# Kernel optimization log

Hardware: AMD Instinct MI355X
Metric: run time of the kernel (lower is better)

Reference implementation:

```python
import jax, jax.numpy as jnp
import numpy as np

BS, H, W, A, NC, G = 2048, 14, 14, 5, 2, 30
SIZE = 1 + NC + 4  # conf, classes, x, y, w, h
OBJ_SCALE, NOOBJ_SCALE, CLASS_SCALE, COORD_SCALE = 5.0, 0.5, 1.0, 1.0


def setup_inputs() -> dict:
    key = jax.random.key(0)
    pred = jax.random.normal(key, (BS, A * SIZE, H, W), dtype=jnp.float32) * 0.5
    # Structured label: G ground-truth boxes per image at distinct cells.
    rng = np.random.default_rng(0)
    lab = np.zeros((BS, 7, H, W), np.float32)
    perm = np.argsort(rng.random((BS, H * W)), axis=1)[:, :G]  # distinct cells
    r, c = perm // W, perm % W
    b = np.arange(BS)[:, None]
    lab[b, 0, r, c] = 1.0
    cls = rng.integers(0, 2, (BS, G)).astype(np.float32)
    lab[b, 1, r, c] = cls
    lab[b, 2, r, c] = 1.0 - cls
    lab[b, 3, r, c] = rng.uniform(0.1, 0.9, (BS, G))  # tx in-cell offset
    lab[b, 4, r, c] = rng.uniform(0.1, 0.9, (BS, G))  # ty
    lab[b, 5, r, c] = rng.uniform(0.05, 0.4, (BS, G))  # tw (normalized)
    lab[b, 6, r, c] = rng.uniform(0.05, 0.4, (BS, G))  # th
    anchors = np.array([[42.0, 44.0], [91.0, 104.0], [162.0, 220.0],
                        [299.0, 170.0], [396.0, 359.0]], np.float32)
    return {"pred": pred, "label": jnp.asarray(lab),
            "anchors": jnp.asarray(anchors), "seen": 6400}


def _yolo_v2_loss(pred, label, anchors, seen):
    f32 = jnp.float32
    anchor_bias = anchors / (512.0 / 14.0) / jnp.array([W, H], f32)  # [A,2], grid-normalized
    # [BS,H,W,A,SIZE]
    pred_r = pred.transpose(0, 2, 3, 1).reshape(BS, H, W, A, SIZE)
    sxy = jax.nn.sigmoid(pred_r[..., 1 + NC:3 + NC])               # sigmoid(x,y)
    ids = jnp.stack(jnp.meshgrid(jnp.arange(W, dtype=f32),
                                 jnp.arange(H, dtype=f32)), -1)[:, :, None, :]  # [H,W,1,2]=(c,r)
    coords = (sxy + ids) / jnp.array([W, H], f32)                  # normalized centers
    wh = jnp.exp(pred_r[..., 3 + NC:5 + NC]) * anchor_bias         # normalized w,h
    boxes = jnp.concatenate([coords, wh], -1)                      # [BS,H,W,A,4]
    aw, ah = anchor_bias[:, 0], anchor_bias[:, 1]

    def per_image(pred_b, sxy_b, boxes_b, label_b):
        obj = label_b[0].reshape(-1)
        vals, flat = jax.lax.top_k(obj, G)
        valid = vals > 0                                           # [G]
        r = flat // W
        c = flat % W
        tx, ty = label_b[3, r, c], label_b[4, r, c]
        tw = jnp.where(valid, label_b[5, r, c], 1.0)
        th = jnp.where(valid, label_b[6, r, c], 1.0)
        # gt boxes are built from detached .data in the torch code -> stop_gradient
        gx = jax.lax.stop_gradient((tx + c.astype(f32)) / W)
        gy = jax.lax.stop_gradient((ty + r.astype(f32)) / H)
        tw = jax.lax.stop_gradient(tw)
        th = jax.lax.stop_gradient(th)
        # pairwise IoU pred boxes [H,W,A] vs gt [G] -> [H,W,A,G]
        x1, y1 = boxes_b[..., 0:1], boxes_b[..., 1:2]
        w1, h1 = boxes_b[..., 2:3], boxes_b[..., 3:4]
        xi1 = jnp.maximum(x1 - 0.5 * w1, gx - 0.5 * tw)
        yi1 = jnp.maximum(y1 - 0.5 * h1, gy - 0.5 * th)
        xi2 = jnp.minimum(x1 + 0.5 * w1, gx + 0.5 * tw)
        yi2 = jnp.minimum(y1 + 0.5 * h1, gy + 0.5 * th)
        inter = jnp.maximum(xi2 - xi1, 0.0) * jnp.maximum(yi2 - yi1, 0.0)
        union = w1 * h1 + tw * th - inter
        iou = jnp.maximum(inter / union, 0.0)
        iou = jnp.where(valid, iou, 0.0)
        noobj = (iou.max(-1) <= 0.6).astype(f32) * (NOOBJ_SCALE * pred_b[..., 0])
        if seen < 12800:
            prior = 0.01 * jnp.concatenate([sxy_b - 0.5,
                                            pred_b[..., 3 + NC:5 + NC]], -1)
        else:
            prior = jnp.zeros((H, W, A, 4), f32)
        coord_obj = jnp.concatenate([prior, noobj[..., None]], -1)  # [H,W,A,5]
        # best anchor per gt (IoU of (0,0,tw,th) vs (0,0,aw,ah))
        ia = jnp.minimum(tw[:, None], aw) * jnp.minimum(th[:, None], ah)
        aid = jnp.argmax(ia / (tw[:, None] * th[:, None] + aw * ah - ia), axis=1)
        wi = (gx * W).astype(jnp.int32)
        fx = gx * W - wi.astype(f32)
        hj = (gy * H).astype(jnp.int32)
        fy = gy * H - hj.astype(f32)
        twh = jnp.log(jnp.stack([tw, th], 1) / anchor_bias[aid])    # [G,2]
        truth_coords = jnp.concatenate([fx[:, None], fy[:, None], twh], 1)
        p_sel = pred_b[hj, wi, aid]                                 # [G,SIZE]
        pc = jnp.concatenate([sxy_b[hj, wi, aid], p_sel[:, 3 + NC:5 + NC]], 1)
        wgt = COORD_SCALE * (2.0 - fx * fy)                         # detached in torch
        closs = wgt[:, None] * (pc - truth_coords)                  # [G,4]
        iou_sel = iou[hj, wi, aid, jnp.arange(G)]                   # [G]
        objl = OBJ_SCALE * (p_sel[:, 0] - iou_sel)
        tco = jnp.concatenate([closs, objl[:, None]], 1) * valid[:, None].astype(f32)
        cvec = jnp.stack([label_b[1, hj, wi], label_b[2, hj, wi]], 1)
        cls_l = CLASS_SCALE * (p_sel[:, 1:1 + NC] - cvec)
        loss_cls = jnp.sum((cls_l ** 2) * valid[:, None].astype(f32))
        m = jnp.zeros((H, W, A), f32).at[hj, wi, aid].add(valid.astype(f32))
        ta = jnp.zeros((H, W, A, 5), f32).at[hj, wi, aid].add(tco)
        m4 = m[..., None]
        comb = m4 * ta + (1.0 - m4) * coord_obj
        il = loss_cls + jnp.sum(comb ** 2)
        return jnp.where(jnp.any(valid), il, 0.0)

    losses = jax.vmap(per_image)(pred_r, sxy, boxes, label)
    return jnp.reshape(jnp.sum(losses) / BS, (1,))


def reference(pred, label, anchors, seen):
    return _yolo_v2_loss(pred, label, anchors, seen)
```

## Files before the change

### kernel.cpp

```cpp
#include <hip/hip_runtime.h>
#include <math.h>

#define BS 2048
#define H_ 14
#define W_ 14
#define A_ 5
#define G_ 30
#define HW_ 196
#define LABN (7 * HW_)
#define LAB4 (LABN / 4)
#define NTH 64
#define NQ 245
#define NBLK (BS * 2)

__device__ __forceinline__ float fast_rcp(float x) { return __builtin_amdgcn_rcpf(x); }

__global__ __launch_bounds__(NTH, 4) void yolo_main(
    const float* __restrict__ pred,
    const float* __restrict__ label,
    const float* __restrict__ anchors,
    float* __restrict__ partial)
{
    __shared__ float  s_lab[LABN];
    __shared__ float4 s_box[G_];
    __shared__ float  s_thr[G_];
    __shared__ float  s_area[G_];
    __shared__ float4 s_tgt[G_];
    __shared__ float4 s_aux[G_];
    __shared__ float  s_aw[A_], s_ah[A_];
    __shared__ int    s_flat[G_];
    __shared__ char   s_map[992] __attribute__((aligned(16)));

    const int blk  = blockIdx.x;
    const int b    = blk >> 1;
    const int half = blk & 1;
    const int lane = threadIdx.x;
    const float* lb = label + (size_t)b * LABN;
    const float* pb = pred  + (size_t)b * (A_ * 7 * HW_);

    {
        const float4* l4 = (const float4*)lb;
        float4* s4 = (float4*)s_lab;
        #pragma unroll
        for (int k = 0; k < 6; ++k) {
            int i = k * NTH + lane;
            if (i < LAB4) s4[i] = l4[i];
        }
    }
    if (lane < 62) ((int4*)s_map)[lane] = make_int4(-1, -1, -1, -1);
    if (lane < A_) {
        const float div1 = 512.0f / 14.0f;
        s_aw[lane] = anchors[2 * lane]     / div1 / (float)W_;
        s_ah[lane] = anchors[2 * lane + 1] / div1 / (float)H_;
    }
    __syncthreads();

    {
        int base = 0;
        #pragma unroll
        for (int k = 0; k < 4; ++k) {
            int idx = k * NTH + lane;
            float v = (idx < HW_) ? s_lab[idx] : 0.0f;
            unsigned long long m = __ballot(v > 0.0f);
            if (v > 0.0f) {
                int rank = base + __popcll(m & ((1ULL << lane) - 1ULL));
                s_flat[rank] = idx;
            }
            base += __popcll(m);
        }
    }
    __syncthreads();

    if (lane < G_) {
        int flat = s_flat[lane];
        int r = flat / W_, c = flat - r * W_;
        float tx = s_lab[3 * HW_ + flat];
        float ty = s_lab[4 * HW_ + flat];
        float tw = s_lab[5 * HW_ + flat];
        float th = s_lab[6 * HW_ + flat];
        float gx = (tx + (float)c) / (float)W_;
        float gy = (ty + (float)r) / (float)H_;
        int   wi = (int)(gx * (float)W_);
        int   hj = (int)(gy * (float)H_);
        float fx = gx * (float)W_ - (float)wi;
        float fy = gy * (float)H_ - (float)hj;
        float best = -1.0f; int aid = 0;
        for (int aa = 0; aa < A_; ++aa) {
            float ia = fminf(tw, s_aw[aa]) * fminf(th, s_ah[aa]);
            float m  = ia / (tw * th + s_aw[aa] * s_ah[aa] - ia);
            if (m > best) { best = m; aid = aa; }
        }
        s_box[lane]  = make_float4(gx - 0.5f * tw, gy - 0.5f * th,
                                   gx + 0.5f * tw, gy + 0.5f * th);
        s_area[lane] = tw * th;
        s_thr[lane]  = 0.375f * tw * th;
        s_tgt[lane]  = make_float4(fx, fy, __logf(tw / s_aw[aid]), __logf(th / s_ah[aid]));
        s_aux[lane]  = make_float4(2.0f - fx * fy,
                                   s_lab[1 * HW_ + hj * W_ + wi],
                                   s_lab[2 * HW_ + hj * W_ + wi],
                                   0.0f);
        s_map[(hj * W_ + wi) * A_ + aid] = (char)lane;
    }
    __syncthreads();

    int  q0   = half * 128 + lane;
    int  q1   = q0 + 64;
    bool act1 = (q1 < NQ);
    int  q1s  = act1 ? q1 : q0;

    float4 P0[2], P1[2], P2[2], P3[2], P4[2], P5[2], P6[2];
    {
        int a0 = q0 / 49, qq = q0 - a0 * 49;
        const float4* p4 = (const float4*)(pb + a0 * 7 * HW_);
        P0[0]=p4[0*49+qq]; P1[0]=p4[1*49+qq]; P2[0]=p4[2*49+qq];
        P3[0]=p4[3*49+qq]; P4[0]=p4[4*49+qq]; P5[0]=p4[5*49+qq]; P6[0]=p4[6*49+qq];
    }
    {
        int a1 = q1s / 49, qq = q1s - a1 * 49;
        const float4* p4 = (const float4*)(pb + a1 * 7 * HW_);
        P0[1]=p4[0*49+qq]; P1[1]=p4[1*49+qq]; P2[1]=p4[2*49+qq];
        P3[1]=p4[3*49+qq]; P4[1]=p4[4*49+qq]; P5[1]=p4[5*49+qq]; P6[1]=p4[6*49+qq];
    }

    float lsum = 0.0f;
    #pragma unroll
    for (int t = 0; t < 2; ++t) {
        bool act = (t == 0) | act1;
        int  q   = t ? q1s : q0;
        int  a   = q / 49;
        int  qq  = q - a * 49;
        int  hw0 = 4 * qq;

        float p0v[4] = {P0[t].x, P0[t].y, P0[t].z, P0[t].w};
        float p1v[4] = {P1[t].x, P1[t].y, P1[t].z, P1[t].w};
        float p2v[4] = {P2[t].x, P2[t].y, P2[t].z, P2[t].w};
        float p3v[4] = {P3[t].x, P3[t].y, P3[t].z, P3[t].w};
        float p4v[4] = {P4[t].x, P4[t].y, P4[t].z, P4[t].w};
        float p5v[4] = {P5[t].x, P5[t].y, P5[t].z, P5[t].w};
        float p6v[4] = {P6[t].x, P6[t].y, P6[t].z, P6[t].w};

        float aw = s_aw[a], ah = s_ah[a];
        float sxv[4], syv[4], xlo[4], xhi[4], ylo[4], yhi[4], acc[4];
        #pragma unroll
        for (int j = 0; j < 4; ++j) {
            int hw = hw0 + j;
            int h  = hw / W_;
            int w  = hw - h * W_;
            float sx = fast_rcp(1.0f + __expf(-p3v[j]));
            float sy = fast_rcp(1.0f + __expf(-p4v[j]));
            float bw = __expf(p5v[j]) * aw;
            float bh = __expf(p6v[j]) * ah;
            float x1 = (sx + (float)w) * (1.0f / (float)W_);
            float y1 = (sy + (float)h) * (1.0f / (float)H_);
            sxv[j] = sx;  syv[j] = sy;
            xlo[j] = x1 - 0.5f * bw;  xhi[j] = x1 + 0.5f * bw;
            ylo[j] = y1 - 0.5f * bh;  yhi[j] = y1 + 0.5f * bh;
            acc[j] = -1e30f;
        }

        #pragma unroll 5
        for (int g = 0; g < G_; ++g) {
            float4 bx  = s_box[g];
            float  thr = s_thr[g];
            #pragma unroll
            for (int j = 0; j < 4; ++j) {
                float xi1 = fmaxf(xlo[j], bx.x);
                float yi1 = fmaxf(ylo[j], bx.y);
                float xi2 = fminf(xhi[j], bx.z);
                float yi2 = fminf(yhi[j], bx.w);
                float dx = fmaxf(xi2 - xi1, 0.0f);
                float dy = fmaxf(yi2 - yi1, 0.0f);
                acc[j] = fmaxf(acc[j], fmaf(dx, dy, -thr));
            }
        }

        if (act) {
            #pragma unroll
            for (int j = 0; j < 4; ++j) {
                int g_at = (int)s_map[(hw0 + j) * A_ + a];
                float area1 = (xhi[j] - xlo[j]) * (yhi[j] - ylo[j]);
                if (g_at >= 0) {
                    float4 tg = s_tgt[g_at];
                    float4 u  = s_aux[g_at];
                    float4 bx = s_box[g_at];
                    float xi1 = fmaxf(xlo[j], bx.x);
                    float yi1 = fmaxf(ylo[j], bx.y);
                    float xi2 = fminf(xhi[j], bx.z);
                    float yi2 = fminf(yhi[j], bx.w);
                    float inter = fmaxf(xi2 - xi1, 0.0f) * fmaxf(yi2 - yi1, 0.0f);
                    float uni   = area1 + s_area[g_at] - inter;
                    float iou   = fmaxf(inter * fast_rcp(uni), 0.0f);
                    float wg = u.x;
                    float d0 = wg * (sxv[j] - tg.x);
                    float d1 = wg * (syv[j] - tg.y);
                    float d2 = wg * (p5v[j] - tg.z);
                    float d3 = wg * (p6v[j] - tg.w);
                    float ob = 5.0f * (p0v[j] - iou);
                    float c1 = p1v[j] - u.y;
                    float c2 = p2v[j] - u.z;
                    lsum += d0*d0 + d1*d1 + d2*d2 + d3*d3 + ob*ob + c1*c1 + c2*c2;
                } else {
                    float pr0 = 0.01f * (sxv[j] - 0.5f);
                    float pr1 = 0.01f * (syv[j] - 0.5f);
                    float pr2 = 0.01f * p5v[j];
                    float pr3 = 0.01f * p6v[j];
                    float no  = (acc[j] <= 0.375f * area1) ? 0.5f * p0v[j] : 0.0f;
                    lsum += pr0*pr0 + pr1*pr1 + pr2*pr2 + pr3*pr3 + no*no;
                }
            }
        }
    }

    #pragma unroll
    for (int off = 32; off > 0; off >>= 1)
        lsum += __shfl_down(lsum, off, 64);
    if (lane == 0) partial[blk] = lsum;
}

__global__ __launch_bounds__(256) void yolo_reduce(
    const float* __restrict__ partial, float* __restrict__ out)
{
    __shared__ float s_red[4];
    const int tid = threadIdx.x, lane = tid & 63, wv = tid >> 6;
    float s = 0.0f;
    for (int i = tid; i < NBLK; i += 256) s += partial[i];
    #pragma unroll
    for (int off = 32; off > 0; off >>= 1)
        s += __shfl_down(s, off, 64);
    if (lane == 0) s_red[wv] = s;
    __syncthreads();
    if (tid == 0) {
        float tot = 0.0f;
        #pragma unroll
        for (int i = 0; i < 4; ++i) tot += s_red[i];
        out[0] = tot * (1.0f / (float)BS);
    }
}

extern "C" void kernel_launch(void* const* d_in, const int* in_sizes, int n_in,
                              void* d_out, int out_size, void* d_ws, size_t ws_size,
                              hipStream_t stream) {
    const float* pred    = (const float*)d_in[0];
    const float* label   = (const float*)d_in[1];
    const float* anchors = (const float*)d_in[2];
    float* out     = (float*)d_out;
    float* partial = (float*)d_ws;

    yolo_main<<<dim3(NBLK), dim3(NTH), 0, stream>>>(pred, label, anchors, partial);
    yolo_reduce<<<dim3(1), dim3(256), 0, stream>>>(partial, out);
}
```

Before: 118.1 us.

## Split per-image setup into its own kernel and fuse final reduction into dense kernel

A separate setup kernel now extracts the ground-truth boxes, targets and the cell/anchor map for each image and writes them to workspace in a struct-of-arrays layout. The dense kernel then runs one 256-thread block per image, reads the box data through scalar/global loads in chunks of 8, and does the last-block reduction itself with an atomic counter, so the separate reduce kernel is gone. This cuts per-block shared-memory label staging and removes one launch, but it adds a memset, a workspace round trip and an extra kernel. Dead code is left behind: an unused yolo_dense kernel and a redundant anchor loop that writes the map twice.

```diff
diff --git a/kernel.cpp b/kernel.cpp
--- a/kernel.cpp
+++ b/kernel.cpp
@@ -8,59 +8,43 @@
 #define G_ 30
 #define HW_ 196
 #define LABN (7 * HW_)
-#define LAB4 (LABN / 4)
-#define NTH 64
 #define NQ 245
-#define NBLK (BS * 2)
+
+#define BM_STRIDE 160
+#define EM_STRIDE 640
+#define BM_OFF   0
+#define EM_OFF   (2u * 1024u * 1024u)
+#define PART_OFF (8u * 1024u * 1024u)
+#define CNT_OFF  (PART_OFF + 16u * 1024u)
 
 __device__ __forceinline__ float fast_rcp(float x) { return __builtin_amdgcn_rcpf(x); }
 
-__global__ __launch_bounds__(NTH, 4) void yolo_main(
-    const float* __restrict__ pred,
+__global__ __launch_bounds__(64) void yolo_setup(
     const float* __restrict__ label,
     const float* __restrict__ anchors,
-    float* __restrict__ partial)
+    float* __restrict__ boxmeta,
+    float* __restrict__ epimeta)
 {
-    __shared__ float  s_lab[LABN];
-    __shared__ float4 s_box[G_];
-    __shared__ float  s_thr[G_];
-    __shared__ float  s_area[G_];
-    __shared__ float4 s_tgt[G_];
-    __shared__ float4 s_aux[G_];
-    __shared__ float  s_aw[A_], s_ah[A_];
-    __shared__ int    s_flat[G_];
-    __shared__ char   s_map[992] __attribute__((aligned(16)));
-
-    const int blk  = blockIdx.x;
-    const int b    = blk >> 1;
-    const int half = blk & 1;
+    __shared__ float s_obj[HW_];
+    __shared__ float s_anch[2 * A_];
+    __shared__ int   s_flat[G_];
+    __shared__ char  s_map[992] __attribute__((aligned(16)));
+
+    const int b    = blockIdx.x;
     const int lane = threadIdx.x;
     const float* lb = label + (size_t)b * LABN;
-    const float* pb = pred  + (size_t)b * (A_ * 7 * HW_);
-
-    {
-        const float4* l4 = (const float4*)lb;
-        float4* s4 = (float4*)s_lab;
-        #pragma unroll
-        for (int k = 0; k < 6; ++k) {
-            int i = k * NTH + lane;
-            if (i < LAB4) s4[i] = l4[i];
-        }
-    }
+
+    if (lane < 49) ((float4*)s_obj)[lane] = ((const float4*)lb)[lane];
+    if (lane < 2 * A_) s_anch[lane] = anchors[lane];
     if (lane < 62) ((int4*)s_map)[lane] = make_int4(-1, -1, -1, -1);
-    if (lane < A_) {
-        const float div1 = 512.0f / 14.0f;
-        s_aw[lane] = anchors[2 * lane]     / div1 / (float)W_;
-        s_ah[lane] = anchors[2 * lane + 1] / div1 / (float)H_;
-    }
     __syncthreads();
 
     {
         int base = 0;
         #pragma unroll
         for (int k = 0; k < 4; ++k) {
-            int idx = k * NTH + lane;
-            float v = (idx < HW_) ? s_lab[idx] : 0.0f;
+            int idx = k * 64 + lane;
+            float v = (idx < HW_) ? s_obj[idx] : 0.0f;
             unsigned long long m = __ballot(v > 0.0f);
             if (v > 0.0f) {
                 int rank = base + __popcll(m & ((1ULL << lane) - 1ULL));
@@ -71,169 +55,290 @@
     }
     __syncthreads();
 
+    float* bm = boxmeta + (size_t)b * BM_STRIDE;
+    float* em = epimeta + (size_t)b * EM_STRIDE;
+
     if (lane < G_) {
         int flat = s_flat[lane];
         int r = flat / W_, c = flat - r * W_;
-        float tx = s_lab[3 * HW_ + flat];
-        float ty = s_lab[4 * HW_ + flat];
-        float tw = s_lab[5 * HW_ + flat];
-        float th = s_lab[6 * HW_ + flat];
+        float tx = lb[3 * HW_ + flat];
+        float ty = lb[4 * HW_ + flat];
+        float tw = lb[5 * HW_ + flat];
+        float th = lb[6 * HW_ + flat];
         float gx = (tx + (float)c) / (float)W_;
         float gy = (ty + (float)r) / (float)H_;
         int   wi = (int)(gx * (float)W_);
         int   hj = (int)(gy * (float)H_);
         float fx = gx * (float)W_ - (float)wi;
         float fy = gy * (float)H_ - (float)hj;
-        float best = -1.0f; int aid = 0;
+        const float div1 = 512.0f / 14.0f;
+        float best = -1.0f; float aw_b = 1.0f, ah_b = 1.0f;
         for (int aa = 0; aa < A_; ++aa) {
-            float ia = fminf(tw, s_aw[aa]) * fminf(th, s_ah[aa]);
-            float m  = ia / (tw * th + s_aw[aa] * s_ah[aa] - ia);
-            if (m > best) { best = m; aid = aa; }
-        }
-        s_box[lane]  = make_float4(gx - 0.5f * tw, gy - 0.5f * th,
-                                   gx + 0.5f * tw, gy + 0.5f * th);
-        s_area[lane] = tw * th;
-        s_thr[lane]  = 0.375f * tw * th;
-        s_tgt[lane]  = make_float4(fx, fy, __logf(tw / s_aw[aid]), __logf(th / s_ah[aid]));
-        s_aux[lane]  = make_float4(2.0f - fx * fy,
-                                   s_lab[1 * HW_ + hj * W_ + wi],
-                                   s_lab[2 * HW_ + hj * W_ + wi],
-                                   0.0f);
+            float aw = s_anch[2 * aa]     / div1 / (float)W_;
+            float ah = s_anch[2 * aa + 1] / div1 / (float)H_;
+            float ia = fminf(tw, aw) * fminf(th, ah);
+            float m  = ia / (tw * th + aw * ah - ia);
+            if (m > best) { best = m; aw_b = aw; ah_b = ah;
+                s_map[(hj * W_ + wi) * A_ + aa] = (char)lane;
+            }
+        }
+        for (int aa = 0; aa < A_; ++aa) s_map[(hj * W_ + wi) * A_ + aa] = (char)-1;
+        float best2 = -1.0f; int aid = 0;
+        for (int aa = 0; aa < A_; ++aa) {
+            float aw = s_anch[2 * aa]     / div1 / (float)W_;
+            float ah = s_anch[2 * aa + 1] / div1 / (float)H_;
+            float ia = fminf(tw, aw) * fminf(th, ah);
+            float m  = ia / (tw * th + aw * ah - ia);
+            if (m > best2) { best2 = m; aid = aa; }
+        }
         s_map[(hj * W_ + wi) * A_ + aid] = (char)lane;
-    }
-    __syncthreads();
-
-    int  q0   = half * 128 + lane;
-    int  q1   = q0 + 64;
-    bool act1 = (q1 < NQ);
-    int  q1s  = act1 ? q1 : q0;
-
-    float4 P0[2], P1[2], P2[2], P3[2], P4[2], P5[2], P6[2];
+
+        float x1 = gx - 0.5f * tw, y1 = gy - 0.5f * th;
+        float x2 = gx + 0.5f * tw, y2 = gy + 0.5f * th;
+        bm[lane]       = x1;
+        bm[32 + lane]  = y1;
+        bm[64 + lane]  = x2;
+        bm[96 + lane]  = y2;
+        bm[128 + lane] = 0.375f * tw * th;
+        ((float4*)em)[lane]         = make_float4(fx, fy, __logf(tw / aw_b), __logf(th / ah_b));
+        ((float4*)(em + 128))[lane] = make_float4(2.0f - fx * fy,
+                                                  lb[1 * HW_ + hj * W_ + wi],
+                                                  lb[2 * HW_ + hj * W_ + wi],
+                                                  tw * th);
+        ((float4*)(em + 256))[lane] = make_float4(x1, y1, x2, y2);
+    } else if (lane < 32) {
+        bm[lane]       = 3e8f;
+        bm[32 + lane]  = 3e8f;
+        bm[64 + lane]  = 3e8f;
+        bm[96 + lane]  = 3e8f;
+        bm[128 + lane] = 3e8f;
+    }
+    __syncthreads();
+    if (lane < 62) ((int4*)(em + 384))[lane] = ((int4*)s_map)[lane];
+}
+
+__global__ __launch_bounds__(256) void yolo_dense(
+    const float* __restrict__ pred,
+    const float* __restrict__ boxmeta,
+    const float* __restrict__ epimeta,
+    float* __restrict__ partial,
+    unsigned int* __restrict__ counter,
+    float* __restrict__ out)
+{
+    __shared__ float4 s_meta[96];
+    __shared__ char   s_map[992] __attribute__((aligned(16)));
+    __shared__ float  s_red[4];
+    __shared__ int    s_last;
+
+    const int b    = blockIdx.x;
+    const int tid  = threadIdx.x;
+    const int lane = tid & 63;
+    const int wv   = tid >> 6;
+    const float* em = epimeta + (size_t)b * EM_STRIDE;
+    const float* bm = boxmeta + (size_t)b * BM_STRIDE;
+    const float* pb = pred + (size_t)b * (A_ * 7 * HW_);
+
+    if (tid < 96) s_meta[tid] = ((const float4*)em)[tid];
+    else if (tid < 158) ((int4*)s_map)[tid - 96] = ((const int4*)(em + 384))[tid - 96];
+
+    const int q  = (tid < NQ) ? tid : NQ - 1;
+    const int a  = q / 49;
+    const int qq = q - a * 49;
+    const int hw0 = 4 * qq;
+    const float4* p4 = (const float4*)(pb + a * 7 * HW_);
+    float4 P0 = p4[0 * 49 + qq];
+    float4 P1 = p4[1 * 49 + qq];
+    float4 P2 = p4[2 * 49 + qq];
+    float4 P3 = p4[3 * 49 + qq];
+    float4 P4 = p4[4 * 49 + qq];
+    float4 P5 = p4[5 * 49 + qq];
+    float4 P6 = p4[6 * 49 + qq];
+    __syncthreads();
+
+    const float div1 = 512.0f / 14.0f;
+    float aw, ah;
     {
-        int a0 = q0 / 49, qq = q0 - a0 * 49;
-        const float4* p4 = (const float4*)(pb + a0 * 7 * HW_);
-        P0[0]=p4[0*49+qq]; P1[0]=p4[1*49+qq]; P2[0]=p4[2*49+qq];
-        P3[0]=p4[3*49+qq]; P4[0]=p4[4*49+qq]; P5[0]=p4[5*49+qq]; P6[0]=p4[6*49+qq];
-    }
+        aw = 0.f; ah = 0.f;
+    }
+
+    float p0v[4] = {P0.x, P0.y, P0.z, P0.w};
+    float p1v[4] = {P1.x, P1.y, P1.z, P1.w};
+    float p2v[4] = {P2.x, P2.y, P2.z, P2.w};
+    float p3v[4] = {P3.x, P3.y, P3.z, P3.w};
+    float p4v[4] = {P4.x, P4.y, P4.z, P4.w};
+    float p5v[4] = {P5.x, P5.y, P5.z, P5.w};
+    float p6v[4] = {P6.x, P6.y, P6.z, P6.w};
+
+    (void)aw; (void)ah;
+
+    float lsum = 0.0f;
+    float sxv[4], syv[4], xlo[4], xhi[4], ylo[4], yhi[4], acc[4];
     {
-        int a1 = q1s / 49, qq = q1s - a1 * 49;
-        const float4* p4 = (const float4*)(pb + a1 * 7 * HW_);
-        P0[1]=p4[0*49+qq]; P1[1]=p4[1*49+qq]; P2[1]=p4[2*49+qq];
-        P3[1]=p4[3*49+qq]; P4[1]=p4[4*49+qq]; P5[1]=p4[5*49+qq]; P6[1]=p4[6*49+qq];
-    }
-
-    float lsum = 0.0f;
+        extern __shared__ float _dummy[]; (void)_dummy;
+    }
+    lsum = 0.0f;
+    if (tid == 0 && b == 0x7fffffff) { partial[0] = P2.x + p0v[0] + p1v[0] + p2v[0] + p3v[0] + p4v[0] + p5v[0] + p6v[0] + sxv[0]*0 + syv[0]*0 + xlo[0]*0 + xhi[0]*0 + ylo[0]*0 + yhi[0]*0 + acc[0]*0 + (float)hw0 + (float)wv + (float)lane; }
+    (void)counter; (void)out; (void)s_last; (void)s_red; (void)bm;
+}
+
+__global__ __launch_bounds__(256) void yolo_dense2(
+    const float* __restrict__ pred,
+    const float* __restrict__ anchors,
+    const float* __restrict__ boxmeta,
+    const float* __restrict__ epimeta,
+    float* __restrict__ partial,
+    unsigned int* __restrict__ counter,
+    float* __restrict__ out)
+{
+    __shared__ float4 s_meta[96];
+    __shared__ char   s_map[992] __attribute__((aligned(16)));
+    __shared__ float  s_red[4];
+    __shared__ int    s_last;
+
+    const int b    = blockIdx.x;
+    const int tid  = threadIdx.x;
+    const int lane = tid & 63;
+    const int wv   = tid >> 6;
+    const float* em = epimeta + (size_t)b * EM_STRIDE;
+    const float* bm = boxmeta + (size_t)b * BM_STRIDE;
+    const float* pb = pred + (size_t)b * (A_ * 7 * HW_);
+
+    if (tid < 96) s_meta[tid] = ((const float4*)em)[tid];
+    else if (tid < 158) ((int4*)s_map)[tid - 96] = ((const int4*)(em + 384))[tid - 96];
+
+    const int q  = (tid < NQ) ? tid : NQ - 1;
+    const int a  = q / 49;
+    const int qq = q - a * 49;
+    const int hw0 = 4 * qq;
+    const float4* p4 = (const float4*)(pb + a * 7 * HW_);
+    float4 P0 = p4[0 * 49 + qq];
+    float4 P1 = p4[1 * 49 + qq];
+    float4 P2 = p4[2 * 49 + qq];
+    float4 P3 = p4[3 * 49 + qq];
+    float4 P4 = p4[4 * 49 + qq];
+    float4 P5 = p4[5 * 49 + qq];
+    float4 P6 = p4[6 * 49 + qq];
+
+    const float div1 = 512.0f / 14.0f;
+    float aw = anchors[2 * a]     / div1 / (float)W_;
+    float ah = anchors[2 * a + 1] / div1 / (float)H_;
+    __syncthreads();
+
+    float p0v[4] = {P0.x, P0.y, P0.z, P0.w};
+    float p1v[4] = {P1.x, P1.y, P1.z, P1.w};
+    float p2v[4] = {P2.x, P2.y, P2.z, P2.w};
+    float p3v[4] = {P3.x, P3.y, P3.z, P3.w};
+    float p4v[4] = {P4.x, P4.y, P4.z, P4.w};
+    float p5v[4] = {P5.x, P5.y, P5.z, P5.w};
+    float p6v[4] = {P6.x, P6.y, P6.z, P6.w};
+
+    float sxv[4], syv[4], xlo[4], xhi[4], ylo[4], yhi[4], acc[4];
     #pragma unroll
-    for (int t = 0; t < 2; ++t) {
-        bool act = (t == 0) | act1;
-        int  q   = t ? q1s : q0;
-        int  a   = q / 49;
-        int  qq  = q - a * 49;
-        int  hw0 = 4 * qq;
-
-        float p0v[4] = {P0[t].x, P0[t].y, P0[t].z, P0[t].w};
-        float p1v[4] = {P1[t].x, P1[t].y, P1[t].z, P1[t].w};
-        float p2v[4] = {P2[t].x, P2[t].y, P2[t].z, P2[t].w};
-        float p3v[4] = {P3[t].x, P3[t].y, P3[t].z, P3[t].w};
-        float p4v[4] = {P4[t].x, P4[t].y, P4[t].z, P4[t].w};
-        float p5v[4] = {P5[t].x, P5[t].y, P5[t].z, P5[t].w};
-        float p6v[4] = {P6[t].x, P6[t].y, P6[t].z, P6[t].w};
-
-        float aw = s_aw[a], ah = s_ah[a];
-        float sxv[4], syv[4], xlo[4], xhi[4], ylo[4], yhi[4], acc[4];
+    for (int j = 0; j < 4; ++j) {
+        int hw = hw0 + j;
+        int h  = hw / W_;
+        int w  = hw - h * W_;
+        float sx = fast_rcp(1.0f + __expf(-p3v[j]));
+        float sy = fast_rcp(1.0f + __expf(-p4v[j]));
+        float bw = __expf(p5v[j]) * aw;
+        float bh = __expf(p6v[j]) * ah;
+        float x1 = (sx + (float)w) * (1.0f / (float)W_);
+        float y1 = (sy + (float)h) * (1.0f / (float)H_);
+        sxv[j] = sx;  syv[j] = sy;
+        xlo[j] = x1 - 0.5f * bw;  xhi[j] = x1 + 0.5f * bw;
+        ylo[j] = y1 - 0.5f * bh;  yhi[j] = y1 + 0.5f * bh;
+        acc[j] = -1e30f;
+    }
+
+    for (int c = 0; c < 4; ++c) {
+        const float* bmc = bm + 8 * c;
+        float X1[8], Y1[8], X2[8], Y2[8], TH[8];
         #pragma unroll
-        for (int j = 0; j < 4; ++j) {
-            int hw = hw0 + j;
-            int h  = hw / W_;
-            int w  = hw - h * W_;
-            float sx = fast_rcp(1.0f + __expf(-p3v[j]));
-            float sy = fast_rcp(1.0f + __expf(-p4v[j]));
-            float bw = __expf(p5v[j]) * aw;
-            float bh = __expf(p6v[j]) * ah;
-            float x1 = (sx + (float)w) * (1.0f / (float)W_);
-            float y1 = (sy + (float)h) * (1.0f / (float)H_);
-            sxv[j] = sx;  syv[j] = sy;
-            xlo[j] = x1 - 0.5f * bw;  xhi[j] = x1 + 0.5f * bw;
-            ylo[j] = y1 - 0.5f * bh;  yhi[j] = y1 + 0.5f * bh;
-            acc[j] = -1e30f;
-        }
-
-        #pragma unroll 5
-        for (int g = 0; g < G_; ++g) {
-            float4 bx  = s_box[g];
-            float  thr = s_thr[g];
+        for (int k = 0; k < 8; ++k) {
+            X1[k] = bmc[k];
+            Y1[k] = bmc[32 + k];
+            X2[k] = bmc[64 + k];
+            Y2[k] = bmc[96 + k];
+            TH[k] = bmc[128 + k];
+        }
+        #pragma unroll
+        for (int k = 0; k < 8; ++k) {
             #pragma unroll
             for (int j = 0; j < 4; ++j) {
-                float xi1 = fmaxf(xlo[j], bx.x);
-                float yi1 = fmaxf(ylo[j], bx.y);
-                float xi2 = fminf(xhi[j], bx.z);
-                float yi2 = fminf(yhi[j], bx.w);
+                float xi1 = fmaxf(xlo[j], X1[k]);
+                float yi1 = fmaxf(ylo[j], Y1[k]);
+                float xi2 = fminf(xhi[j], X2[k]);
+                float yi2 = fminf(yhi[j], Y2[k]);
                 float dx = fmaxf(xi2 - xi1, 0.0f);
                 float dy = fmaxf(yi2 - yi1, 0.0f);
-                acc[j] = fmaxf(acc[j], fmaf(dx, dy, -thr));
+                acc[j] = fmaxf(acc[j], fmaf(dx, dy, -TH[k]));
             }
         }
-
-        if (act) {
-            #pragma unroll
-            for (int j = 0; j < 4; ++j) {
-                int g_at = (int)s_map[(hw0 + j) * A_ + a];
-                float area1 = (xhi[j] - xlo[j]) * (yhi[j] - ylo[j]);
-                if (g_at >= 0) {
-                    float4 tg = s_tgt[g_at];
-                    float4 u  = s_aux[g_at];
-                    float4 bx = s_box[g_at];
-                    float xi1 = fmaxf(xlo[j], bx.x);
-                    float yi1 = fmaxf(ylo[j], bx.y);
-                    float xi2 = fminf(xhi[j], bx.z);
-                    float yi2 = fminf(yhi[j], bx.w);
-                    float inter = fmaxf(xi2 - xi1, 0.0f) * fmaxf(yi2 - yi1, 0.0f);
-                    float uni   = area1 + s_area[g_at] - inter;
-                    float iou   = fmaxf(inter * fast_rcp(uni), 0.0f);
-                    float wg = u.x;
-                    float d0 = wg * (sxv[j] - tg.x);
-                    float d1 = wg * (syv[j] - tg.y);
-                    float d2 = wg * (p5v[j] - tg.z);
-                    float d3 = wg * (p6v[j] - tg.w);
-                    float ob = 5.0f * (p0v[j] - iou);
-                    float c1 = p1v[j] - u.y;
-                    float c2 = p2v[j] - u.z;
-                    lsum += d0*d0 + d1*d1 + d2*d2 + d3*d3 + ob*ob + c1*c1 + c2*c2;
-                } else {
-                    float pr0 = 0.01f * (sxv[j] - 0.5f);
-                    float pr1 = 0.01f * (syv[j] - 0.5f);
-                    float pr2 = 0.01f * p5v[j];
-                    float pr3 = 0.01f * p6v[j];
-                    float no  = (acc[j] <= 0.375f * area1) ? 0.5f * p0v[j] : 0.0f;
-                    lsum += pr0*pr0 + pr1*pr1 + pr2*pr2 + pr3*pr3 + no*no;
-                }
-            }
-        }
-    }
+    }
+
+    float lsum = 0.0f;
+    const float4* s_tgt  = s_meta;
+    const float4* s_aux  = s_meta + 32;
+    const float4* s_ebox = s_meta + 64;
+    #pragma unroll
+    for (int j = 0; j < 4; ++j) {
+        int g_at = (int)s_map[(hw0 + j) * A_ + a];
+        float area1 = (xhi[j] - xlo[j]) * (yhi[j] - ylo[j]);
+        if (g_at >= 0) {
+            float4 tg = s_tgt[g_at];
+            float4 u  = s_aux[g_at];
+            float4 bx = s_ebox[g_at];
+            float xi1 = fmaxf(xlo[j], bx.x);
+            float yi1 = fmaxf(ylo[j], bx.y);
+            float xi2 = fminf(xhi[j], bx.z);
+            float yi2 = fminf(yhi[j], bx.w);
+            float inter = fmaxf(xi2 - xi1, 0.0f) * fmaxf(yi2 - yi1, 0.0f);
+            float uni   = area1 + u.w - inter;
+            float iou   = fmaxf(inter * fast_rcp(uni), 0.0f);
+            float wg = u.x;
+            float d0 = wg * (sxv[j] - tg.x);
+            float d1 = wg * (syv[j] - tg.y);
+            float d2 = wg * (p5v[j] - tg.z);
+            float d3 = wg * (p6v[j] - tg.w);
+            float ob = 5.0f * (p0v[j] - iou);
+            float c1 = p1v[j] - u.y;
+            float c2 = p2v[j] - u.z;
+            lsum += d0*d0 + d1*d1 + d2*d2 + d3*d3 + ob*ob + c1*c1 + c2*c2;
+        } else {
+            float pr0 = 0.01f * (sxv[j] - 0.5f);
+            float pr1 = 0.01f * (syv[j] - 0.5f);
+            float pr2 = 0.01f * p5v[j];
+            float pr3 = 0.01f * p6v[j];
+            float no  = (acc[j] <= 0.375f * area1) ? 0.5f * p0v[j] : 0.0f;
+            lsum += pr0*pr0 + pr1*pr1 + pr2*pr2 + pr3*pr3 + no*no;
+        }
+    }
+    if (tid >= NQ) lsum = 0.0f;
 
     #pragma unroll
     for (int off = 32; off > 0; off >>= 1)
         lsum += __shfl_down(lsum, off, 64);
-    if (lane == 0) partial[blk] = lsum;
-}
-
-__global__ __launch_bounds__(256) void yolo_reduce(
-    const float* __restrict__ partial, float* __restrict__ out)
-{
-    __shared__ float s_red[4];
-    const int tid = threadIdx.x, lane = tid & 63, wv = tid >> 6;
-    float s = 0.0f;
-    for (int i = tid; i < NBLK; i += 256) s += partial[i];
-    #pragma unroll
-    for (int off = 32; off > 0; off >>= 1)
-        s += __shfl_down(s, off, 64);
-    if (lane == 0) s_red[wv] = s;
+    if (lane == 0) s_red[wv] = lsum;
     __syncthreads();
     if (tid == 0) {
-        float tot = 0.0f;
+        float tot = s_red[0] + s_red[1] + s_red[2] + s_red[3];
+        partial[b] = tot;
+        __threadfence();
+        unsigned int old = atomicAdd(counter, 1u);
+        s_last = (old == (unsigned int)(BS - 1)) ? 1 : 0;
+    }
+    __syncthreads();
+    if (s_last) {
+        __threadfence();
+        float s = 0.0f;
+        for (int i = tid; i < BS; i += 256) s += partial[i];
         #pragma unroll
-        for (int i = 0; i < 4; ++i) tot += s_red[i];
-        out[0] = tot * (1.0f / (float)BS);
+        for (int off = 32; off > 0; off >>= 1)
+            s += __shfl_down(s, off, 64);
+        if (lane == 0) s_red[wv] = s;
+        __syncthreads();
+        if (tid == 0)
+            out[0] = (s_red[0] + s_red[1] + s_red[2] + s_red[3]) * (1.0f / (float)BS);
     }
 }
 
@@ -243,9 +348,16 @@
     const float* pred    = (const float*)d_in[0];
     const float* label   = (const float*)d_in[1];
     const float* anchors = (const float*)d_in[2];
-    float* out     = (float*)d_out;
-    float* partial = (float*)d_ws;
-
-    yolo_main<<<dim3(NBLK), dim3(NTH), 0, stream>>>(pred, label, anchors, partial);
-    yolo_reduce<<<dim3(1), dim3(256), 0, stream>>>(partial, out);
+    float* out = (float*)d_out;
+
+    char* ws = (char*)d_ws;
+    float*        boxmeta = (float*)(ws + BM_OFF);
+    float*        epimeta = (float*)(ws + EM_OFF);
+    float*        partial = (float*)(ws + PART_OFF);
+    unsigned int* counter = (unsigned int*)(ws + CNT_OFF);
+
+    hipMemsetAsync(counter, 0, sizeof(unsigned int), stream);
+    yolo_setup<<<dim3(BS), dim3(64), 0, stream>>>(label, anchors, boxmeta, epimeta);
+    yolo_dense2<<<dim3(BS), dim3(256), 0, stream>>>(pred, anchors, boxmeta, epimeta,
+                                                    partial, counter, out);
 }
```

Result: slower. 164.7 us (+39.5%).
